# Optimization experiments

Measured on AMD Instinct MI355X. Metric: run time of the kernel, lower is better.

The kernel has to match this reference:

```python
import jax, jax.numpy as jnp
import numpy as np

KH = KW = 3
STRIDE = 1
PAD = 1
DIL = 1


def setup_inputs() -> dict:
    key = jax.random.key(0)
    k1, k2, k3, k4 = jax.random.split(key, 4)
    B, C, H, W = 16, 64, 64, 64
    Cout = 64
    K = KH * KW
    x = jax.random.normal(k1, (B, C, H, W), jnp.float32)
    offset = jax.random.normal(k2, (B, 2 * K, H, W), jnp.float32)
    mask = jax.random.uniform(k3, (B, K, H, W), jnp.float32)
    # uniform(-stdv, stdv) init with stdv = 1/sqrt(C*KH*KW) ~ 0.0417; scaled normal is close enough
    weight = jax.random.normal(k4, (Cout, C, KH, KW), jnp.float32) * 0.04
    bias = jnp.zeros((Cout,), jnp.float32)  # no_bias=True -> frozen zeros, still added
    return dict(input=x, offset=offset, mask=mask, weight=weight, bias=bias)


def _bilinear(img, py, px):
    # img: [C, H, W]; py, px: [K, Ho, Wo] float sampling coords
    # DCNv2 semantics: out-of-bounds corner contributions are zero.
    H, W = img.shape[1], img.shape[2]
    y0f = jnp.floor(py)
    x0f = jnp.floor(px)
    wy = py - y0f
    wx = px - x0f
    y0 = y0f.astype(jnp.int32)
    x0 = x0f.astype(jnp.int32)
    out = jnp.zeros((img.shape[0],) + py.shape, img.dtype)
    for dy in (0, 1):
        for dx in (0, 1):
            yi = y0 + dy
            xi = x0 + dx
            valid = ((yi >= 0) & (yi < H) & (xi >= 0) & (xi < W)).astype(img.dtype)
            v = img[:, jnp.clip(yi, 0, H - 1), jnp.clip(xi, 0, W - 1)]  # [C,K,Ho,Wo]
            w = (wy if dy else 1.0 - wy) * (wx if dx else 1.0 - wx)
            out = out + v * (w * valid)[None]
    return out  # [C, K, Ho, Wo]


def reference(input, offset, mask, weight, bias):
    B, C, H, W = input.shape
    Cout, _, kh, kw = weight.shape
    K = kh * kw
    Ho = (H + 2 * PAD - (DIL * (kh - 1) + 1)) // STRIDE + 1
    Wo = (W + 2 * PAD - (DIL * (kw - 1) + 1)) // STRIDE + 1
    off = offset.reshape(B, K, 2, Ho, Wo)  # per kernel point: (dy, dx)
    ky = jnp.repeat(jnp.arange(kh), kw)  # [K] kernel row index
    kx = jnp.tile(jnp.arange(kw), kh)    # [K] kernel col index
    base_y = jnp.arange(Ho) * STRIDE - PAD
    base_x = jnp.arange(Wo) * STRIDE - PAD
    py = off[:, :, 0] + (base_y[None, None, :, None] + (ky * DIL)[None, :, None, None])
    px = off[:, :, 1] + (base_x[None, None, None, :] + (kx * DIL)[None, :, None, None])
    sampled = jax.vmap(_bilinear)(input, py, px)        # [B, C, K, Ho, Wo]
    modulated = sampled * mask[:, None]                 # mask-modulated accumulation
    out = jnp.einsum('bckpq,ock->bopq', modulated, weight.reshape(Cout, C, K))
    return out + bias[None, :, None, None]
```

## Files before the change

kernel.cpp:

```cpp
#include <hip/hip_runtime.h>
#include <hip/hip_fp16.h>

#define BATCH 16
#define C_IN  64
#define HH    64
#define WW    64
#define COUT  64
#define KK    9
#define HW    4096
#define CK    576
#define MROW  200
#define WROWS 13
#define WLO   6

typedef _Float16 f16x8 __attribute__((ext_vector_type(8)));
typedef float    f32x4 __attribute__((ext_vector_type(4)));

__device__ __forceinline__ unsigned short f32_to_f16u(float f) {
    _Float16 h = (_Float16)f;
    unsigned short u;
    __builtin_memcpy(&u, &h, 2);
    return u;
}

__device__ __forceinline__ __half2 as_h2(unsigned int u) {
    __half2 r; __builtin_memcpy(&r, &u, 4); return r;
}
__device__ __forceinline__ unsigned int as_u32(__half2 v) {
    unsigned int u; __builtin_memcpy(&u, &v, 4); return u;
}

__global__ __launch_bounds__(256) void prep_kernel(
    const float* __restrict__ x, const float* __restrict__ w,
    unsigned short* __restrict__ xt, unsigned short* __restrict__ wt) {
    __shared__ unsigned short tile[64][72];
    const int t = threadIdx.x;
    const int blk = blockIdx.x;
    if (blk < 1024) {
        const int b = blk >> 6, y = blk & 63;
        const float* xrow = x + ((b * 64) * 64 + y) * 64;
#pragma unroll
        for (int it = 0; it < 4; ++it) {
            const int idx = it * 256 + t;
            const int c = idx >> 4, seg = idx & 15;
            const float4 v = *(const float4*)(xrow + c * HW + seg * 4);
            tile[seg * 4 + 0][c] = f32_to_f16u(v.x);
            tile[seg * 4 + 1][c] = f32_to_f16u(v.y);
            tile[seg * 4 + 2][c] = f32_to_f16u(v.z);
            tile[seg * 4 + 3][c] = f32_to_f16u(v.w);
        }
        __syncthreads();
#pragma unroll
        for (int it = 0; it < 2; ++it) {
            const int idx = it * 256 + t;
            const int xx = idx >> 3, cs = idx & 7;
            *(int4*)&xt[((b * HW) + y * 64 + xx) * 64 + cs * 8] =
                *(const int4*)&tile[xx][cs * 8];
        }
    } else {
        const int i = (blk - 1024) * 256 + t;
        const int j = i & 7;
        const int l = (i >> 3) & 63;
        const int ot = (i >> 9) & 3;
        const int r = i >> 11;
        const int ks = r % 6, kc = r / 6;
        const int o  = ot * 16 + (l & 15);
        const int kk = ks * 32 + (l >> 4) * 8 + j;
        const int tap = kk >> 6, c = kk & 63;
        const int k = kc * 3 + tap;
        wt[i] = f32_to_f16u(w[o * CK + c * KK + k]);
    }
}

__global__ __launch_bounds__(256, 1) void dcn_main_kernel(
    const float* __restrict__ offset, const float* __restrict__ mask,
    const unsigned short* __restrict__ xt, const unsigned short* __restrict__ wt,
    const float* __restrict__ bias, float* __restrict__ out) {
    __shared__ __align__(16) unsigned short win[WROWS * 64 * 64];
    __shared__ __align__(16) unsigned short Mlds[4][16 * MROW];
    __shared__ __align__(16) int PWw[576 * 4];
    __shared__ __align__(8) unsigned short PWa[576 * 4];
    __shared__ __align__(8) unsigned short PWg[576 * 4];

    const int t    = threadIdx.x;
    const int wave = __builtin_amdgcn_readfirstlane(t >> 6);
    const int lane = t & 63;
    const int quad = lane >> 4, m16 = lane & 15;

    const int blk = blockIdx.x;
    const int xcd = blk & 7;
    const int i7  = blk >> 3;
    const int b   = (xcd << 1) | (i7 >> 6);
    const int row = i7 & 63;
    const int qbase = wave * 16;

    const float* offb = offset + b * (2 * KK * HW) + row * 64;
    const float* mb   = mask + b * (KK * HW) + row * 64;
    const char* xtb   = (const char*)(xt + b * (HW * 64));

    float oyv[3], oxv[3], mkv[3];
#pragma unroll
    for (int p = 0; p < 3; ++p) {
        const int it = p * 256 + t;
        if (it < 576) {
            const int tap = it >> 6, q = it & 63;
            oyv[p] = offb[(2 * tap) * HW + q];
            oxv[p] = offb[(2 * tap + 1) * HW + q];
            mkv[p] = mb[tap * HW + q];
        } else { oyv[p] = 0.f; oxv[p] = 0.f; mkv[p] = 0.f; }
    }
    asm volatile("" :: "v"(oyv[0]), "v"(oxv[0]), "v"(mkv[0]),
                       "v"(oyv[1]), "v"(oxv[1]), "v"(mkv[1]),
                       "v"(oyv[2]), "v"(oxv[2]), "v"(mkv[2]));

#pragma unroll
    for (int s = 0; s < 2 * WROWS; ++s) {
        const int slot = s >> 1;
        const int srcrow = min(max(row - WLO + slot, 0), HH - 1);
        const char* src = xtb + srcrow * 8192 + (s & 1) * 4096 + t * 16;
        __builtin_amdgcn_global_load_lds(
            (const __attribute__((address_space(1))) unsigned int*)src,
            (__attribute__((address_space(3))) unsigned int*)
                ((char*)win + s * 4096 + t * 16),
            16, 0, 0);
    }
    __builtin_amdgcn_sched_barrier(0);

#pragma unroll
    for (int p = 0; p < 3; ++p) {
        const int it = p * 256 + t;
        if (it < 576) {
            const int tap = it >> 6, q = it & 63;
            const int ky = (tap * 11) >> 5;
            const int kx = tap - ky * 3;
            const float py  = oyv[p] + (float)(row - 1 + ky);
            const float pxf = oxv[p] + (float)(q - 1 + kx);
            const float y0f = floorf(py), x0f = floorf(pxf);
            const float wy = py - y0f, wx = pxf - x0f;
            const int y0 = (int)y0f, x0 = (int)x0f;
            const int y1 = y0 + 1,   x1 = x0 + 1;
            const float vy0 = (y0 >= 0 && y0 < HH) ? 1.f : 0.f;
            const float vy1 = (y1 >= 0 && y1 < HH) ? 1.f : 0.f;
            const float vx0 = (x0 >= 0 && x0 < WW) ? 1.f : 0.f;
            const float vx1 = (x1 >= 0 && x1 < WW) ? 1.f : 0.f;
            const float mk = mkv[p];
            const float w00 = (1.f - wy) * (1.f - wx) * vy0 * vx0 * mk;
            const float w01 = (1.f - wy) * wx         * vy0 * vx1 * mk;
            const float w10 = wy * (1.f - wx)         * vy1 * vx0 * mk;
            const float w11 = wy * wx                 * vy1 * vx1 * mk;
            const int cy0 = min(max(y0, 0), HH - 1), cy1 = min(max(y1, 0), HH - 1);
            const int cx0 = min(max(x0, 0), WW - 1), cx1 = min(max(x1, 0), WW - 1);
            const int sl0 = cy0 - (row - WLO);
            const int sl1 = cy1 - (row - WLO);
            const int esc = (sl0 < 0) | (sl1 > (WROWS - 1));
            const int c0 = min(max(sl0, 0), WROWS - 1);
            const int c1 = min(max(sl1, 0), WROWS - 1);
            const unsigned int s00 = f32_to_f16u(w00);
            const unsigned int s01 = f32_to_f16u(w01);
            const unsigned int s10 = f32_to_f16u(w10);
            const unsigned int s11 = f32_to_f16u(w11);
            int4 P0;
            P0.x = (int)(s00 | (s00 << 16));
            P0.y = (int)(s01 | (s01 << 16));
            P0.z = (int)(s10 | (s10 << 16));
            P0.w = (int)(s11 | (s11 << 16));
            *(int4*)&PWw[it * 4] = P0;
            ushort4 A;
            A.x = (unsigned short)((c0 * 64 + cx0) | (esc << 15));
            A.y = (unsigned short)(c0 * 64 + cx1);
            A.z = (unsigned short)(c1 * 64 + cx0);
            A.w = (unsigned short)(c1 * 64 + cx1);
            *(ushort4*)&PWa[it * 4] = A;
            ushort4 G;
            G.x = (unsigned short)(cy0 * 64 + cx0);
            G.y = (unsigned short)(cy0 * 64 + cx1);
            G.z = (unsigned short)(cy1 * 64 + cx0);
            G.w = (unsigned short)(cy1 * 64 + cx1);
            *(ushort4*)&PWg[it * 4] = G;
        }
    }
    __syncthreads();

    f32x4 acc[4];
#pragma unroll
    for (int ot = 0; ot < 4; ++ot)
#pragma unroll
        for (int r = 0; r < 4; ++r) acc[ot][r] = 0.f;

    char* MW = (char*)Mlds[wave];
    const int lg  = lane >> 3;
    const int co2 = (lane & 7) * 16;

#pragma unroll
    for (int kc = 0; kc < 3; ++kc) {
#pragma unroll
        for (int i = 0; i < 6; ++i) {
            const int l  = i * 8 + lg;
            const int it = (3 * kc + (l >> 4)) * 64 + qbase + (l & 15);
            const ushort4 a = *(const ushort4*)&PWa[it * 4];
            const int4 p0   = *(const int4*)&PWw[it * 4];
            uint4 q0 = *(const uint4*)((const char*)win + (((int)a.x & 0x7FFF) << 7) + co2);
            uint4 q1 = *(const uint4*)((const char*)win + (((int)a.y) << 7) + co2);
            uint4 q2 = *(const uint4*)((const char*)win + (((int)a.z) << 7) + co2);
            uint4 q3 = *(const uint4*)((const char*)win + (((int)a.w) << 7) + co2);
            const bool esc = (a.x & 0x8000u) != 0;
            if (__builtin_expect(__any(esc), 0)) {
                if (esc) {
                    const ushort4 ga = *(const ushort4*)&PWg[it * 4];
                    q0 = *(const uint4*)(xtb + ((int)ga.x << 7) + co2);
                    q1 = *(const uint4*)(xtb + ((int)ga.y << 7) + co2);
                    q2 = *(const uint4*)(xtb + ((int)ga.z << 7) + co2);
                    q3 = *(const uint4*)(xtb + ((int)ga.w << 7) + co2);
                }
            }
            const __half2 c00 = as_h2((unsigned)p0.x);
            const __half2 c01 = as_h2((unsigned)p0.y);
            const __half2 c10 = as_h2((unsigned)p0.z);
            const __half2 c11 = as_h2((unsigned)p0.w);
            uint4 ov;
            {
                __half2 v = __hmul2(c00, as_h2(q0.x));
                v = __hfma2(c01, as_h2(q1.x), v);
                v = __hfma2(c10, as_h2(q2.x), v);
                v = __hfma2(c11, as_h2(q3.x), v);
                ov.x = as_u32(v);
            }
            {
                __half2 v = __hmul2(c00, as_h2(q0.y));
                v = __hfma2(c01, as_h2(q1.y), v);
                v = __hfma2(c10, as_h2(q2.y), v);
                v = __hfma2(c11, as_h2(q3.y), v);
                ov.y = as_u32(v);
            }
            {
                __half2 v = __hmul2(c00, as_h2(q0.z));
                v = __hfma2(c01, as_h2(q1.z), v);
                v = __hfma2(c10, as_h2(q2.z), v);
                v = __hfma2(c11, as_h2(q3.z), v);
                ov.z = as_u32(v);
            }
            {
                __half2 v = __hmul2(c00, as_h2(q0.w));
                v = __hfma2(c01, as_h2(q1.w), v);
                v = __hfma2(c10, as_h2(q2.w), v);
                v = __hfma2(c11, as_h2(q3.w), v);
                ov.w = as_u32(v);
            }
            *(uint4*)(MW + (l & 15) * 400 + (l >> 4) * 128 + co2) = ov;
        }
        const unsigned short* wkc = wt + kc * (6 * 4 * 512);
#pragma unroll
        for (int ks = 0; ks < 6; ++ks) {
            const f16x8 bfrag =
                *(const f16x8*)(MW + m16 * 400 + ks * 64 + quad * 16);
#pragma unroll
            for (int ot = 0; ot < 4; ++ot) {
                const f16x8 afrag =
                    *(const f16x8*)(wkc + (ks * 4 + ot) * 512 + lane * 8);
                acc[ot] = __builtin_amdgcn_mfma_f32_16x16x32_f16(afrag, bfrag,
                                                                 acc[ot], 0, 0, 0);
            }
        }
    }

    float* ob = out + b * (COUT * HW) + row * 64 + qbase + m16;
#pragma unroll
    for (int ot = 0; ot < 4; ++ot)
#pragma unroll
        for (int r = 0; r < 4; ++r) {
            const int o = ot * 16 + quad * 4 + r;
            ob[o * HW] = acc[ot][r] + bias[o];
        }
}

extern "C" void kernel_launch(void* const* d_in, const int* in_sizes, int n_in,
                              void* d_out, int out_size, void* d_ws,
                              size_t ws_size, hipStream_t stream) {
    const float* x    = (const float*)d_in[0];
    const float* off  = (const float*)d_in[1];
    const float* mask = (const float*)d_in[2];
    const float* w    = (const float*)d_in[3];
    const float* bias = (const float*)d_in[4];
    float* out = (float*)d_out;

    unsigned short* xt = (unsigned short*)d_ws;
    unsigned short* wt = (unsigned short*)((char*)d_ws + 8388608);

    prep_kernel<<<1024 + 144, 256, 0, stream>>>(x, w, xt, wt);
    dcn_main_kernel<<<1024, 256, 0, stream>>>(off, mask, xt, wt, bias, out);
}
```

Measured before the change: 108.7 us.

## Process two output rows per block and gather bilinear samples directly into MFMA fragments

Each block now covers two output rows with 512 threads, sharing one 13-row input window in LDS so the total window traffic per output row is lower. The window is stored with an XOR swizzle to spread LDS bank accesses. Each lane builds its MFMA B fragment in registers straight from the bilinear gather, which removes the per-wave LDS staging buffer and the extra write/read round trip. Window-escape handling now recomputes coordinates from global offsets instead of keeping a precomputed table. The costs are a larger block with fewer blocks and heavier register and LDS use per block.

```diff
diff --git a/kernel.cpp b/kernel.cpp
--- a/kernel.cpp
+++ b/kernel.cpp
@@ -9,9 +9,8 @@
 #define KK    9
 #define HW    4096
 #define CK    576
-#define MROW  200
 #define WROWS 13
-#define WLO   6
+#define WLO   5
 
 typedef _Float16 f16x8 __attribute__((ext_vector_type(8)));
 typedef float    f32x4 __attribute__((ext_vector_type(4)));
@@ -72,68 +71,75 @@
     }
 }
 
-__global__ __launch_bounds__(256, 1) void dcn_main_kernel(
+__global__ __launch_bounds__(512, 1) void dcn_main_kernel(
     const float* __restrict__ offset, const float* __restrict__ mask,
     const unsigned short* __restrict__ xt, const unsigned short* __restrict__ wt,
     const float* __restrict__ bias, float* __restrict__ out) {
-    __shared__ __align__(16) unsigned short win[WROWS * 64 * 64];
-    __shared__ __align__(16) unsigned short Mlds[4][16 * MROW];
-    __shared__ __align__(16) int PWw[576 * 4];
-    __shared__ __align__(8) unsigned short PWa[576 * 4];
-    __shared__ __align__(8) unsigned short PWg[576 * 4];
+    __shared__ __align__(16) unsigned short win[WROWS * 4096];
+    __shared__ __align__(16) int PWw[2][576 * 4];
+    __shared__ __align__(16) unsigned int PWa[2][576 * 4];
 
     const int t    = threadIdx.x;
     const int wave = __builtin_amdgcn_readfirstlane(t >> 6);
     const int lane = t & 63;
     const int quad = lane >> 4, m16 = lane & 15;
+    const int rw   = wave >> 2;
+    const int qb   = (wave & 3) * 16;
 
     const int blk = blockIdx.x;
     const int xcd = blk & 7;
-    const int i7  = blk >> 3;
-    const int b   = (xcd << 1) | (i7 >> 6);
-    const int row = i7 & 63;
-    const int qbase = wave * 16;
-
-    const float* offb = offset + b * (2 * KK * HW) + row * 64;
-    const float* mb   = mask + b * (KK * HW) + row * 64;
+    const int i6  = blk >> 3;
+    const int b   = (xcd << 1) | (i6 >> 5);
+    const int R   = (i6 & 31) * 2;
+    const int base = R - WLO;
+
+    const float* offb = offset + b * (2 * KK * HW);
+    const float* mb   = mask + b * (KK * HW);
     const char* xtb   = (const char*)(xt + b * (HW * 64));
 
     float oyv[3], oxv[3], mkv[3];
 #pragma unroll
     for (int p = 0; p < 3; ++p) {
-        const int it = p * 256 + t;
-        if (it < 576) {
-            const int tap = it >> 6, q = it & 63;
-            oyv[p] = offb[(2 * tap) * HW + q];
-            oxv[p] = offb[(2 * tap + 1) * HW + q];
-            mkv[p] = mb[tap * HW + q];
+        const int it = p * 512 + t;
+        if (it < 1152) {
+            const int rsel = it >= 576;
+            const int j = it - rsel * 576;
+            const int tap = j >> 6, q = j & 63;
+            const int rowX = R + rsel;
+            oyv[p] = offb[(2 * tap) * HW + rowX * 64 + q];
+            oxv[p] = offb[(2 * tap + 1) * HW + rowX * 64 + q];
+            mkv[p] = mb[tap * HW + rowX * 64 + q];
         } else { oyv[p] = 0.f; oxv[p] = 0.f; mkv[p] = 0.f; }
     }
     asm volatile("" :: "v"(oyv[0]), "v"(oxv[0]), "v"(mkv[0]),
                        "v"(oyv[1]), "v"(oxv[1]), "v"(mkv[1]),
                        "v"(oyv[2]), "v"(oxv[2]), "v"(mkv[2]));
 
-#pragma unroll
-    for (int s = 0; s < 2 * WROWS; ++s) {
-        const int slot = s >> 1;
-        const int srcrow = min(max(row - WLO + slot, 0), HH - 1);
-        const char* src = xtb + srcrow * 8192 + (s & 1) * 4096 + t * 16;
+    const int pxl = t >> 3;
+    const int swb = ((t & 7) ^ (pxl & 7)) << 4;
+#pragma unroll
+    for (int s = 0; s < WROWS; ++s) {
+        const int srcrow = min(max(base + s, 0), HH - 1);
+        const char* src = xtb + srcrow * 8192 + pxl * 128 + swb;
         __builtin_amdgcn_global_load_lds(
             (const __attribute__((address_space(1))) unsigned int*)src,
             (__attribute__((address_space(3))) unsigned int*)
-                ((char*)win + s * 4096 + t * 16),
+                ((char*)win + s * 8192 + t * 16),
             16, 0, 0);
     }
     __builtin_amdgcn_sched_barrier(0);
 
 #pragma unroll
     for (int p = 0; p < 3; ++p) {
-        const int it = p * 256 + t;
-        if (it < 576) {
-            const int tap = it >> 6, q = it & 63;
+        const int it = p * 512 + t;
+        if (it < 1152) {
+            const int rsel = it >= 576;
+            const int j = it - rsel * 576;
+            const int tap = j >> 6, q = j & 63;
+            const int rowX = R + rsel;
             const int ky = (tap * 11) >> 5;
             const int kx = tap - ky * 3;
-            const float py  = oyv[p] + (float)(row - 1 + ky);
+            const float py  = oyv[p] + (float)(rowX - 1 + ky);
             const float pxf = oxv[p] + (float)(q - 1 + kx);
             const float y0f = floorf(py), x0f = floorf(pxf);
             const float wy = py - y0f, wx = pxf - x0f;
@@ -150,11 +156,12 @@
             const float w11 = wy * wx                 * vy1 * vx1 * mk;
             const int cy0 = min(max(y0, 0), HH - 1), cy1 = min(max(y1, 0), HH - 1);
             const int cx0 = min(max(x0, 0), WW - 1), cx1 = min(max(x1, 0), WW - 1);
-            const int sl0 = cy0 - (row - WLO);
-            const int sl1 = cy1 - (row - WLO);
-            const int esc = (sl0 < 0) | (sl1 > (WROWS - 1));
+            const int sl0 = cy0 - base, sl1 = cy1 - base;
+            const unsigned esc = (sl0 < 0) | (sl1 > (WROWS - 1));
             const int c0 = min(max(sl0, 0), WROWS - 1);
             const int c1 = min(max(sl1, 0), WROWS - 1);
+            const int wl00 = c0 * 64 + cx0, wl01 = c0 * 64 + cx1;
+            const int wl10 = c1 * 64 + cx0, wl11 = c1 * 64 + cx1;
             const unsigned int s00 = f32_to_f16u(w00);
             const unsigned int s01 = f32_to_f16u(w01);
             const unsigned int s10 = f32_to_f16u(w10);
@@ -164,19 +171,13 @@
             P0.y = (int)(s01 | (s01 << 16));
             P0.z = (int)(s10 | (s10 << 16));
             P0.w = (int)(s11 | (s11 << 16));
-            *(int4*)&PWw[it * 4] = P0;
-            ushort4 A;
-            A.x = (unsigned short)((c0 * 64 + cx0) | (esc << 15));
-            A.y = (unsigned short)(c0 * 64 + cx1);
-            A.z = (unsigned short)(c1 * 64 + cx0);
-            A.w = (unsigned short)(c1 * 64 + cx1);
-            *(ushort4*)&PWa[it * 4] = A;
-            ushort4 G;
-            G.x = (unsigned short)(cy0 * 64 + cx0);
-            G.y = (unsigned short)(cy0 * 64 + cx1);
-            G.z = (unsigned short)(cy1 * 64 + cx0);
-            G.w = (unsigned short)(cy1 * 64 + cx1);
-            *(ushort4*)&PWg[it * 4] = G;
+            *(int4*)&PWw[rsel][j * 4] = P0;
+            uint4 A;
+            A.x = (unsigned)((wl00 << 7) | ((wl00 & 7) << 4)) | (esc << 31);
+            A.y = (unsigned)((wl01 << 7) | ((wl01 & 7) << 4));
+            A.z = (unsigned)((wl10 << 7) | ((wl10 & 7) << 4));
+            A.w = (unsigned)((wl11 << 7) | ((wl11 & 7) << 4));
+            *(uint4*)&PWa[rsel][j * 4] = A;
         }
     }
     __syncthreads();
@@ -187,30 +188,42 @@
 #pragma unroll
         for (int r = 0; r < 4; ++r) acc[ot][r] = 0.f;
 
-    char* MW = (char*)Mlds[wave];
-    const int lg  = lane >> 3;
-    const int co2 = (lane & 7) * 16;
+    const char* winc = (const char*)win;
+    const int rowX = R + rw;
 
 #pragma unroll
     for (int kc = 0; kc < 3; ++kc) {
-#pragma unroll
-        for (int i = 0; i < 6; ++i) {
-            const int l  = i * 8 + lg;
-            const int it = (3 * kc + (l >> 4)) * 64 + qbase + (l & 15);
-            const ushort4 a = *(const ushort4*)&PWa[it * 4];
-            const int4 p0   = *(const int4*)&PWw[it * 4];
-            uint4 q0 = *(const uint4*)((const char*)win + (((int)a.x & 0x7FFF) << 7) + co2);
-            uint4 q1 = *(const uint4*)((const char*)win + (((int)a.y) << 7) + co2);
-            uint4 q2 = *(const uint4*)((const char*)win + (((int)a.z) << 7) + co2);
-            uint4 q3 = *(const uint4*)((const char*)win + (((int)a.w) << 7) + co2);
-            const bool esc = (a.x & 0x8000u) != 0;
-            if (__builtin_expect(__any(esc), 0)) {
-                if (esc) {
-                    const ushort4 ga = *(const ushort4*)&PWg[it * 4];
-                    q0 = *(const uint4*)(xtb + ((int)ga.x << 7) + co2);
-                    q1 = *(const uint4*)(xtb + ((int)ga.y << 7) + co2);
-                    q2 = *(const uint4*)(xtb + ((int)ga.z << 7) + co2);
-                    q3 = *(const uint4*)(xtb + ((int)ga.w << 7) + co2);
+        const unsigned short* wkc = wt + kc * (6 * 4 * 512);
+#pragma unroll
+        for (int ks = 0; ks < 6; ++ks) {
+            const int tap = kc * 3 + (ks >> 1);
+            const int it  = tap * 64 + qb + m16;
+            const uint4 A  = *(const uint4*)&PWa[rw][it * 4];
+            const int4  p0 = *(const int4*)&PWw[rw][it * 4];
+            const unsigned sswz = (unsigned)(((ks & 1) * 4 + quad) << 4);
+            uint4 q0 = *(const uint4*)(winc + ((A.x & 0x7FFFFFFFu) ^ sswz));
+            uint4 q1 = *(const uint4*)(winc + (A.y ^ sswz));
+            uint4 q2 = *(const uint4*)(winc + (A.z ^ sswz));
+            uint4 q3 = *(const uint4*)(winc + (A.w ^ sswz));
+            if (__builtin_expect(__any((int)(A.x >> 31)), 0)) {
+                if (A.x >> 31) {
+                    const int q = qb + m16;
+                    const int ky = (tap * 11) >> 5;
+                    const int kx = tap - ky * 3;
+                    const float oy = offb[(2 * tap) * HW + rowX * 64 + q];
+                    const float ox = offb[(2 * tap + 1) * HW + rowX * 64 + q];
+                    const float py  = oy + (float)(rowX - 1 + ky);
+                    const float pxf = ox + (float)(q - 1 + kx);
+                    const int y0 = (int)floorf(py), x0 = (int)floorf(pxf);
+                    const int cy0 = min(max(y0, 0), HH - 1);
+                    const int cy1 = min(max(y0 + 1, 0), HH - 1);
+                    const int cx0 = min(max(x0, 0), WW - 1);
+                    const int cx1 = min(max(x0 + 1, 0), WW - 1);
+                    const int hoff = (ks & 1) * 64 + quad * 16;
+                    q0 = *(const uint4*)(xtb + ((cy0 * 64 + cx0) << 7) + hoff);
+                    q1 = *(const uint4*)(xtb + ((cy0 * 64 + cx1) << 7) + hoff);
+                    q2 = *(const uint4*)(xtb + ((cy1 * 64 + cx0) << 7) + hoff);
+                    q3 = *(const uint4*)(xtb + ((cy1 * 64 + cx1) << 7) + hoff);
                 }
             }
             const __half2 c00 = as_h2((unsigned)p0.x);
@@ -246,13 +259,8 @@
                 v = __hfma2(c11, as_h2(q3.w), v);
                 ov.w = as_u32(v);
             }
-            *(uint4*)(MW + (l & 15) * 400 + (l >> 4) * 128 + co2) = ov;
-        }
-        const unsigned short* wkc = wt + kc * (6 * 4 * 512);
-#pragma unroll
-        for (int ks = 0; ks < 6; ++ks) {
-            const f16x8 bfrag =
-                *(const f16x8*)(MW + m16 * 400 + ks * 64 + quad * 16);
+            f16x8 bfrag;
+            __builtin_memcpy(&bfrag, &ov, 16);
 #pragma unroll
             for (int ot = 0; ot < 4; ++ot) {
                 const f16x8 afrag =
@@ -263,7 +271,7 @@
         }
     }
 
-    float* ob = out + b * (COUT * HW) + row * 64 + qbase + m16;
+    float* ob = out + b * (COUT * HW) + rowX * 64 + qb + m16;
 #pragma unroll
     for (int ot = 0; ot < 4; ++ot)
 #pragma unroll
@@ -287,5 +295,5 @@
     unsigned short* wt = (unsigned short*)((char*)d_ws + 8388608);
 
     prep_kernel<<<1024 + 144, 256, 0, stream>>>(x, w, xt, wt);
-    dcn_main_kernel<<<1024, 256, 0, stream>>>(off, mask, xt, wt, bias, out);
-}
+    dcn_main_kernel<<<512, 512, 0, stream>>>(off, mask, xt, wt, bias, out);
+}
```

Result: faster. 96.92 us, median of 2 (-10.9%).
